# Performance work log

Hardware: AMD Instinct MI355X
Metric: run time of the kernel (lower is better)

Reference implementation:

```python
import jax, jax.numpy as jnp
import numpy as np

TEMPERATURE = 0.8
TOP_K = 50
TOP_P = 0.9
REP_PENALTY = 1.2
NEG_INF = -1000000000.0


def setup_inputs() -> dict:
    key = jax.random.key(0)
    k1, k2 = jax.random.split(key)
    B, S, V, L = 64, 8, 50257, 2048
    logits = jax.random.normal(k1, (B, S, V), dtype=jnp.float32)
    input_ids = jax.random.randint(k2, (B, L), 0, V, dtype=jnp.int64)
    return {"logits": logits, "input_ids": input_ids}


def _modify_logits(logits, input_ids):
    B, S, V = logits.shape
    # temperature scale
    x = logits / TEMPERATURE
    # top-k: keep values >= k-th largest (ties negligible for random floats)
    kth = jax.lax.top_k(x, TOP_K)[0][..., -1:]  # [B,S,1]
    x = jnp.where(x >= kth, x, NEG_INF)
    # top-p nucleus filtering
    order = jnp.argsort(-x, axis=-1)                       # descending order indices
    sorted_logits = jnp.take_along_axis(x, order, axis=-1)
    cum = jnp.cumsum(jax.nn.softmax(sorted_logits, axis=-1), axis=-1)
    remove = cum > TOP_P
    # shift right by one; always keep the top token
    remove = jnp.concatenate([jnp.zeros_like(remove[..., :1]), remove[..., :-1]], axis=-1)
    inv = jnp.argsort(order, axis=-1)                      # inverse permutation
    remove_orig = jnp.take_along_axis(remove, inv, axis=-1)
    x = jnp.where(remove_orig, NEG_INF, x)
    # repetition penalty on last position only, for tokens present in history
    present = jnp.zeros((B, V), dtype=bool).at[
        jnp.arange(B)[:, None], input_ids
    ].set(True)
    last = x[:, -1, :]
    penalized = jnp.where(last < 0, last * REP_PENALTY, last / REP_PENALTY)
    last = jnp.where(present, penalized, last)
    return x.at[:, -1, :].set(last)


def reference(logits, input_ids):
    return _modify_logits(logits, input_ids)
```

## Files before the change

kernel.cpp:

```cpp
#include <hip/hip_runtime.h>
#include <stdint.h>

#define V 50257
#define B_ 64
#define S_ 8
#define ROWS (B_ * S_)
#define L_ 2048
#define NEG_INF -1000000000.0f
#define PEN_NEG (-1200000000.0f)
#define MASK_WORDS_PER_B 1571
#define TOTAL (ROWS * V)
#define NVEC (TOTAL / 4)
#define TOP_CAP 64
#define TRAW 2.8f
#define GBLK_F4 1571
#define GBLOCKS_G ((NVEC + GBLK_F4 - 1) / GBLK_F4)
#define GCAP_BLK 64
#define CAPROW 512

#define WS_BCNT    0
#define WS_GCAND   16384
#define WS_NEED    (WS_GCAND + (size_t)GBLOCKS_G * GCAP_BLK * 8)
#define WS_ROWPARAM 0
#define WS_MASK     8192

__device__ __forceinline__ unsigned fkey(float f) {
    unsigned u = __float_as_uint(f);
    return (u & 0x80000000u) ? ~u : (u | 0x80000000u);
}

__device__ __forceinline__ int blockReduceSum256(int v, int tid, int* s4) {
#pragma unroll
    for (int off = 32; off; off >>= 1) v += __shfl_down(v, off);
    __syncthreads();
    if ((tid & 63) == 0) s4[tid >> 6] = v;
    __syncthreads();
    return s4[0] + s4[1] + s4[2] + s4[3];
}


__global__ __launch_bounds__(256) void prep_kernel(const float4* __restrict__ in4,
                                                   uint2* __restrict__ gcand,
                                                   unsigned* __restrict__ bcnt) {
    const int blk = blockIdx.x;
    const int tid = threadIdx.x;
    const int start = blk * GBLK_F4;
    const int end = min(start + GBLK_F4, NVEC);

    __shared__ uint2 buf[GCAP_BLK];
    __shared__ int lcnt, s_of;
    if (tid == 0) { lcnt = 0; s_of = 0; }
    __syncthreads();

    const int i0 = start + tid;
    const float4* p0 = in4 + min(i0,            NVEC - 1);
    const float4* p1 = in4 + min(i0 + 256,      NVEC - 1);
    const float4* p2 = in4 + min(i0 + 2 * 256,  NVEC - 1);
    const float4* p3 = in4 + min(i0 + 3 * 256,  NVEC - 1);
    const float4* p4 = in4 + min(i0 + 4 * 256,  NVEC - 1);
    const float4* p5 = in4 + min(i0 + 5 * 256,  NVEC - 1);
    const float4* p6 = in4 + min(i0 + 6 * 256,  NVEC - 1);

    float4 va0, va1, va2, va3, va4, va5, va6;
    asm volatile("global_load_dwordx4 %0, %1, off" : "=v"(va0) : "v"(p0));
    asm volatile("global_load_dwordx4 %0, %1, off" : "=v"(va1) : "v"(p1));
    asm volatile("global_load_dwordx4 %0, %1, off" : "=v"(va2) : "v"(p2));
    asm volatile("global_load_dwordx4 %0, %1, off" : "=v"(va3) : "v"(p3));
    asm volatile("global_load_dwordx4 %0, %1, off" : "=v"(va4) : "v"(p4));
    asm volatile("global_load_dwordx4 %0, %1, off" : "=v"(va5) : "v"(p5));
    asm volatile("global_load_dwordx4 %0, %1, off" : "=v"(va6) : "v"(p6));

    asm volatile("s_waitcnt vmcnt(0)" ::: "memory");
    __builtin_amdgcn_sched_barrier(0);

    float c0v = 0.f, c1v = 0.f, c2v = 0.f, c3v = 0.f, c4v = 0.f;
    int c0i = 0, c1i = 0, c2i = 0, c3i = 0, c4i = 0;
    int nh = 0;

#define INS(val, ei)                                                          \
    if ((val) >= TRAW) {                                                      \
        c4v = c3v; c4i = c3i; c3v = c2v; c3i = c2i; c2v = c1v; c2i = c1i;     \
        c1v = c0v; c1i = c0i; c0v = (val); c0i = (ei); ++nh;                  \
    }
#define CONSUME(vv, kk)                                                       \
    {                                                                         \
        int i = i0 + (kk) * 256;                                              \
        if (i < end) {                                                        \
            int e = i << 2;                                                   \
            INS((vv).x, e)                                                    \
            INS((vv).y, e + 1)                                                \
            INS((vv).z, e + 2)                                                \
            INS((vv).w, e + 3)                                                \
        }                                                                     \
    }
    CONSUME(va0, 0) CONSUME(va1, 1) CONSUME(va2, 2) CONSUME(va3, 3)
    CONSUME(va4, 4) CONSUME(va5, 5) CONSUME(va6, 6)
#undef CONSUME
#undef INS

    if (nh > 0) {
        int m = nh > 5 ? 5 : nh;
        if (nh > 5) s_of = 1;
        int base = atomicAdd(&lcnt, m);
        if (m >= 1 && base + 0 < GCAP_BLK) buf[base + 0] = make_uint2((unsigned)c0i, __float_as_uint(c0v));
        if (m >= 2 && base + 1 < GCAP_BLK) buf[base + 1] = make_uint2((unsigned)c1i, __float_as_uint(c1v));
        if (m >= 3 && base + 2 < GCAP_BLK) buf[base + 2] = make_uint2((unsigned)c2i, __float_as_uint(c2v));
        if (m >= 4 && base + 3 < GCAP_BLK) buf[base + 3] = make_uint2((unsigned)c3i, __float_as_uint(c3v));
        if (m >= 5 && base + 4 < GCAP_BLK) buf[base + 4] = make_uint2((unsigned)c4i, __float_as_uint(c4v));
    }
    __syncthreads();
    if (tid == 0) bcnt[blk] = s_of ? 1000000u : (unsigned)lcnt;
    int take = min(lcnt, GCAP_BLK);
    for (int j = tid; j < take; j += 256) gcand[(size_t)blk * GCAP_BLK + j] = buf[j];
}


__global__ __launch_bounds__(256) void select_kernel(const float* __restrict__ logits,
                                                     const int* __restrict__ ids,
                                                     const uint2* __restrict__ gcand,
                                                     const unsigned* __restrict__ bcnt,
                                                     float* __restrict__ out) {
    const int row = blockIdx.x;
    const int tid = threadIdx.x;
    __shared__ float cX[CAPROW];
    __shared__ unsigned cR[CAPROW];
    __shared__ int cI[CAPROW];
    __shared__ float sVal[TOP_CAP];
    __shared__ int sIdx[TOP_CAP];
    __shared__ double sExp[TOP_CAP];
    __shared__ unsigned presRow[MASK_WORDS_PER_B];
    __shared__ int s_c, s_M, s_bad, s_ti;
    __shared__ float s_t;
    __shared__ int s_red[4];

    const float* rp = logits + (size_t)row * V;
    const unsigned e0 = (unsigned)row * (unsigned)V;
    if (tid == 0) { s_c = 0; s_bad = 0; }
    __syncthreads();

    {
        const int b0 = (int)((e0 >> 2) / GBLK_F4);
        const int b1 = (int)(((e0 + V - 1) >> 2) / GBLK_F4);
        for (int blk = b0; blk <= b1; ++blk) {
            unsigned c = bcnt[blk];
            if (c > GCAP_BLK && tid == 0) s_bad = 1;
            int take = min((int)c, GCAP_BLK);
            for (int j = tid; j < take; j += 256) {
                uint2 u = gcand[(size_t)blk * GCAP_BLK + j];
                if (u.x / (unsigned)V == (unsigned)row) {
                    int p = atomicAdd(&s_c, 1);
                    if (p < CAPROW) {
                        cR[p] = u.y;
                        cX[p] = __uint_as_float(u.y) / 0.8f;
                        cI[p] = (int)(u.x - e0);
                    }
                }
            }
        }
    }
    __syncthreads();
    int cnt = s_c;
    if (s_bad || cnt < 50 || cnt > CAPROW) {
        unsigned lo = 0u, hi = 0xFFFFFFFFu;
        while (lo < hi) {
            unsigned mid = lo + ((hi - lo) >> 1) + 1u;
            int c = 0;
            for (int j = tid; j < V; j += 256) c += (int)(fkey(rp[j]) >= mid);
            c = blockReduceSum256(c, tid, s_red);
            if (c >= 50) lo = mid; else hi = mid - 1u;
        }
        unsigned gl = (lo > 2u) ? lo - 2u : 0u;
        __syncthreads();
        if (tid == 0) s_c = 0;
        __syncthreads();
        for (int j = tid; j < V; j += 256) {
            float v = rp[j];
            if (fkey(v) >= gl) {
                int p = atomicAdd(&s_c, 1);
                if (p < CAPROW) { cR[p] = __float_as_uint(v); cX[p] = v / 0.8f; cI[p] = j; }
            }
        }
        __syncthreads();
        cnt = min(s_c, CAPROW);
    }

    if (tid < TOP_CAP) { sVal[tid] = -3.4e38f; sIdx[tid] = 0x7FFFFFFF; }
    __syncthreads();

    {
        float v0 = -3.4e38f, v1 = -3.4e38f;
        int i0 = 0x7FFFFFFF, i1 = 0x7FFFFFFF;
        if (tid < cnt) { v0 = cX[tid]; i0 = cI[tid]; }
        if (tid + 256 < cnt) { v1 = cX[tid + 256]; i1 = cI[tid + 256]; }
        int r0 = 0, r1 = 0;
        for (int j = 0; j < cnt; ++j) {
            float w = cX[j];
            int wi = cI[j];
            r0 += (w > v0) || (w == v0 && wi < i0);
            r1 += (w > v1) || (w == v1 && wi < i1);
        }
        if (tid < cnt && r0 < TOP_CAP) { sVal[r0] = v0; sIdx[r0] = i0; }
        if (tid + 256 < cnt && r1 < TOP_CAP) { sVal[r1] = v1; sIdx[r1] = i1; }
    }
    __syncthreads();

    if (tid == 0) {
        float kth = sVal[49];
        int M = 50;
        while (M < TOP_CAP && sVal[M] == kth) ++M;
        s_M = M;
    }
    __syncthreads();
    int M = s_M;
    if (tid < M) sExp[tid] = exp((double)sVal[tid] - (double)sVal[0]);
    __syncthreads();
    if (tid == 0) {
        double denom = 0.0;
        for (int i = 0; i < M; ++i) denom += sExp[i];
        double cum = 0.0;
        int J = M - 1;
        for (int i = 0; i < M; ++i) {
            cum += sExp[i] / denom;
            if (cum > 0.9) { J = i; break; }
        }
        s_t = sVal[J];
        s_ti = sIdx[J];
    }

    const bool pen = (row & 7) == 7;
    if (pen) {
        __syncthreads();
        for (int w = tid; w < MASK_WORDS_PER_B; w += 256) presRow[w] = 0u;
        __syncthreads();
        const int* bp = ids + (row >> 3) * L_;
#pragma unroll
        for (int k = 0; k < L_ / 256; ++k) {
            int t = bp[k * 256 + tid];
            atomicOr(&presRow[t >> 5], 1u << (t & 31));
        }
    }
    __syncthreads();

    float* orow = out + (size_t)row * V;
    const unsigned mis = (unsigned)(((size_t)row * (size_t)V) & 3u);
    const int a0 = (int)((4u - mis) & 3u);
    const int nv = (V - a0) >> 2;
    const int tailStart = a0 + (nv << 2);
    if (tid < a0) {
        int t = tid;
        orow[t] = (pen && ((presRow[t >> 5] >> (t & 31)) & 1u)) ? PEN_NEG : NEG_INF;
    }
    if (tid < V - tailStart) {
        int t = tailStart + tid;
        orow[t] = (pen && ((presRow[t >> 5] >> (t & 31)) & 1u)) ? PEN_NEG : NEG_INF;
    }
    float4* ob = reinterpret_cast<float4*>(orow + a0);
    if (!pen) {
        const float4 bg = make_float4(NEG_INF, NEG_INF, NEG_INF, NEG_INF);
        for (int j = tid; j < nv; j += 256) ob[j] = bg;
    } else {
        for (int j = tid; j < nv; j += 256) {
            int t = a0 + (j << 2);
            float4 bg;
            bg.x = ((presRow[t >> 5]       >> (t & 31))       & 1u) ? PEN_NEG : NEG_INF;
            bg.y = ((presRow[(t+1) >> 5]   >> ((t+1) & 31))   & 1u) ? PEN_NEG : NEG_INF;
            bg.z = ((presRow[(t+2) >> 5]   >> ((t+2) & 31))   & 1u) ? PEN_NEG : NEG_INF;
            bg.w = ((presRow[(t+3) >> 5]   >> ((t+3) & 31))   & 1u) ? PEN_NEG : NEG_INF;
            ob[j] = bg;
        }
    }
    __syncthreads();

    float t = s_t;
    int tie = s_ti;
    for (int j = tid; j < cnt; j += 256) {
        float x = cX[j];
        int tok = cI[j];
        bool keep = (x > t) || (x == t && tok <= tie);
        if (keep) {
            float oo = x;
            if (pen && ((presRow[tok >> 5] >> (tok & 31)) & 1u))
                oo = (oo < 0.0f) ? oo * 1.2f : oo * (1.0f / 1.2f);
            orow[tok] = oo;
        }
    }
}

#define CAND_CAP 4096
#define RT_THREADS 1024

__global__ __launch_bounds__(256) void mask_only_kernel(const int* __restrict__ ids,
                                                        unsigned* __restrict__ mask) {
    const int tid = threadIdx.x;
    const int b = blockIdx.x;
    __shared__ unsigned lds[MASK_WORDS_PER_B];
    for (int w = tid; w < MASK_WORDS_PER_B; w += 256) lds[w] = 0u;
    __syncthreads();
    const int* bp = ids + b * L_;
#pragma unroll
    for (int k = 0; k < L_ / 256; ++k) {
        int t = bp[k * 256 + tid];
        atomicOr(&lds[t >> 5], 1u << (t & 31));
    }
    __syncthreads();
    unsigned* mp = mask + b * MASK_WORDS_PER_B;
    for (int w = tid; w < MASK_WORDS_PER_B; w += 256) mp[w] = lds[w];
}

__global__ __launch_bounds__(RT_THREADS, 8) void row_thresh_kernel(
        const float* __restrict__ logits, uint4* __restrict__ rowParam) {
    const int tid = threadIdx.x;
    const int row = blockIdx.x;
    if (row >= ROWS) return;
    const float* rp = logits + (size_t)row * V;

    __shared__ float candV[CAND_CAP];
    __shared__ int   candI[CAND_CAP];
    __shared__ float sVal[TOP_CAP];
    __shared__ int   sIdx[TOP_CAP];
    __shared__ double sExp[TOP_CAP];
    __shared__ int s_cnt, s_M;
    __shared__ int s_red[RT_THREADS / 64];

    const unsigned mis = (unsigned)(((size_t)row * (size_t)V) & 3u);
    const int a0 = (int)((4u - mis) & 3u);
    const int nv = (V - a0) >> 2;
    const int tailStart = a0 + (nv << 2);
    const float4* vp = reinterpret_cast<const float4*>(rp + a0);

    float TR = 2.4f;
    int cnt = 0;
    for (int attempt = 0; attempt < 12; ++attempt) {
        if (tid == 0) s_cnt = 0;
        __syncthreads();
        for (int base = tid; base < nv; base += 4 * RT_THREADS) {
            int i1 = base + RT_THREADS, i2 = base + 2 * RT_THREADS, i3 = base + 3 * RT_THREADS;
            float4 a = vp[base];
            float4 b = vp[i1 < nv ? i1 : nv - 1];
            float4 c = vp[i2 < nv ? i2 : nv - 1];
            float4 d = vp[i3 < nv ? i3 : nv - 1];
            float va[16] = {a.x, a.y, a.z, a.w, b.x, b.y, b.z, b.w,
                            c.x, c.y, c.z, c.w, d.x, d.y, d.z, d.w};
            int ib[4] = {base, i1, i2, i3};
            bool ok[4] = {true, i1 < nv, i2 < nv, i3 < nv};
#pragma unroll
            for (int q = 0; q < 4; ++q) {
                if (!ok[q]) continue;
#pragma unroll
                for (int cc = 0; cc < 4; ++cc) {
                    float v = va[q * 4 + cc];
                    if (v >= TR) {
                        int p = atomicAdd(&s_cnt, 1);
                        if (p < CAND_CAP) { candV[p] = v / 0.8f; candI[p] = a0 + (ib[q] << 2) + cc; }
                    }
                }
            }
        }
        if (tid < a0) {
            float v = rp[tid];
            if (v >= TR) {
                int p = atomicAdd(&s_cnt, 1);
                if (p < CAND_CAP) { candV[p] = v / 0.8f; candI[p] = tid; }
            }
        }
        if (tid < V - tailStart) {
            float v = rp[tailStart + tid];
            if (v >= TR) {
                int p = atomicAdd(&s_cnt, 1);
                if (p < CAND_CAP) { candV[p] = v / 0.8f; candI[p] = tailStart + tid; }
            }
        }
        __syncthreads();
        cnt = s_cnt;
        if (cnt >= 50 && cnt <= CAND_CAP) break;
        if (cnt < 50) TR -= 1.2f; else TR += 1.2f;
        __syncthreads();
    }
    if (cnt > CAND_CAP) cnt = CAND_CAP;

    if (tid < TOP_CAP) { sVal[tid] = -3.4e38f; sIdx[tid] = 0x7FFFFFFF; }
    __syncthreads();

    {
        float v0 = (tid < cnt) ? candV[tid] : -3.4e38f;
        int i0 = (tid < cnt) ? candI[tid] : 0x7FFFFFFF;
        float v1 = (tid + RT_THREADS < cnt) ? candV[tid + RT_THREADS] : -3.4e38f;
        int i1 = (tid + RT_THREADS < cnt) ? candI[tid + RT_THREADS] : 0x7FFFFFFF;
        float v2 = (tid + 2 * RT_THREADS < cnt) ? candV[tid + 2 * RT_THREADS] : -3.4e38f;
        int i2 = (tid + 2 * RT_THREADS < cnt) ? candI[tid + 2 * RT_THREADS] : 0x7FFFFFFF;
        float v3 = (tid + 3 * RT_THREADS < cnt) ? candV[tid + 3 * RT_THREADS] : -3.4e38f;
        int i3 = (tid + 3 * RT_THREADS < cnt) ? candI[tid + 3 * RT_THREADS] : 0x7FFFFFFF;
        int r0 = 0, r1 = 0, r2 = 0, r3 = 0;
        for (int j = 0; j < cnt; ++j) {
            float w = candV[j];
            int wi = candI[j];
            r0 += (w > v0) || (w == v0 && wi < i0);
            r1 += (w > v1) || (w == v1 && wi < i1);
            r2 += (w > v2) || (w == v2 && wi < i2);
            r3 += (w > v3) || (w == v3 && wi < i3);
        }
        if (tid < cnt && r0 < TOP_CAP) { sVal[r0] = v0; sIdx[r0] = i0; }
        if (tid + RT_THREADS < cnt && r1 < TOP_CAP) { sVal[r1] = v1; sIdx[r1] = i1; }
        if (tid + 2 * RT_THREADS < cnt && r2 < TOP_CAP) { sVal[r2] = v2; sIdx[r2] = i2; }
        if (tid + 3 * RT_THREADS < cnt && r3 < TOP_CAP) { sVal[r3] = v3; sIdx[r3] = i3; }
    }
    __syncthreads();

    if (tid == 0) {
        float kth = sVal[49];
        int M = 50;
        while (M < TOP_CAP && sVal[M] == kth) ++M;
        s_M = M;
    }
    __syncthreads();
    int M = s_M;
    if (tid < M) sExp[tid] = exp((double)sVal[tid] - (double)sVal[0]);
    __syncthreads();

    if (tid == 0) {
        double denom = 0.0;
#pragma unroll 1
        for (int i = 0; i < M; ++i) denom += sExp[i];
        double cum = 0.0;
        int J = M - 1;
#pragma unroll 1
        for (int i = 0; i < M; ++i) {
            cum += sExp[i] / denom;
            if (cum > 0.9) { J = i; break; }
        }
        float t = sVal[J];
        float w = t * 0.8f;
        unsigned wb = __float_as_uint(w);
        unsigned lo = 0xFFFFFFFFu, hi = 0u;
        for (int d = -4; d <= 4; ++d) {
            unsigned ub = wb + (unsigned)d;
            if (__uint_as_float(ub) / 0.8f == t) { if (ub < lo) lo = ub; if (ub > hi) hi = ub; }
        }
        rowParam[row] = make_uint4(lo, hi, (unsigned)sIdx[J], 0u);
    }
}

__global__ __launch_bounds__(256) void apply_kernel(const float4* __restrict__ in4,
                                                    const uint4* __restrict__ rowParam,
                                                    const unsigned* __restrict__ mask,
                                                    float4* __restrict__ out4) {
    int gid = blockIdx.x * 256 + threadIdx.x;
    int i0 = gid << 1;
    if (i0 >= NVEC) return;
    float4 a = in4[i0];
    float4 b = in4[i0 + 1];
    unsigned e = (unsigned)i0 << 2;
    unsigned row = e / (unsigned)V;
    unsigned tok0 = e - row * (unsigned)V;
    uint4 p0 = rowParam[row];
    bool crosses = (tok0 + 7u >= (unsigned)V);
    uint4 p1 = crosses ? rowParam[row + 1] : p0;
    float xs[8] = {a.x, a.y, a.z, a.w, b.x, b.y, b.z, b.w};
    float o[8];
#pragma unroll
    for (int c = 0; c < 8; ++c) {
        unsigned tok = tok0 + (unsigned)c;
        unsigned r = row;
        uint4 pp = p0;
        if (tok >= (unsigned)V) { tok -= (unsigned)V; r = row + 1u; pp = p1; }
        float v = xs[c];
        float vlo = __uint_as_float(pp.x);
        float vhi = __uint_as_float(pp.y);
        bool keep = (v > vhi) || (v >= vlo && tok <= pp.z);
        float oo = keep ? v * 1.25f : NEG_INF;
        if ((r & 7u) == 7u) {
            unsigned w = mask[(r >> 3) * MASK_WORDS_PER_B + (tok >> 5)];
            if ((w >> (tok & 31u)) & 1u) oo = (oo < 0.0f) ? oo * 1.2f : oo * (1.0f / 1.2f);
        }
        o[c] = oo;
    }
    out4[i0] = make_float4(o[0], o[1], o[2], o[3]);
    out4[i0 + 1] = make_float4(o[4], o[5], o[6], o[7]);
}

extern "C" void kernel_launch(void* const* d_in, const int* in_sizes, int n_in,
                              void* d_out, int out_size, void* d_ws, size_t ws_size,
                              hipStream_t stream) {
    const float* logits = (const float*)d_in[0];
    const int* ids = (const int*)d_in[1];
    float* out = (float*)d_out;

    if (ws_size >= WS_NEED) {
        unsigned* bcnt = (unsigned*)((char*)d_ws + WS_BCNT);
        uint2* gcand = (uint2*)((char*)d_ws + WS_GCAND);
        prep_kernel<<<GBLOCKS_G, 256, 0, stream>>>((const float4*)logits, gcand, bcnt);
        select_kernel<<<ROWS, 256, 0, stream>>>(logits, ids, gcand, bcnt, out);
    } else {
        uint4* rowParam = (uint4*)((char*)d_ws + WS_ROWPARAM);
        unsigned* mask = (unsigned*)((char*)d_ws + WS_MASK);
        mask_only_kernel<<<B_, 256, 0, stream>>>(ids, mask);
        row_thresh_kernel<<<ROWS, RT_THREADS, 0, stream>>>(logits, rowParam);
        apply_kernel<<<(NVEC / 2 + 255) / 256, 256, 0, stream>>>((const float4*)logits, rowParam,
                                                                 mask, (float4*)out);
    }
}
```

Baseline: 57.46 us.

## Replace block-level candidate gather with per-wave chunks and shuffle prefix scan

The threshold prefilter now assigns each wavefront its own contiguous chunk and compacts candidates with a wave-level shuffle prefix sum, writing directly to global memory with a per-wave count. This removes the shared-memory atomics, the block barrier and the staging copy of the previous block-wide gather. The select kernel reads the per-wave counts into shared memory and scans candidate slots in one flattened loop. The cost is more count entries and slots to scan per row, with a smaller per-wave cap (32) that may trigger the slow fallback more often.

```diff
diff --git a/kernel.cpp b/kernel.cpp
--- a/kernel.cpp
+++ b/kernel.cpp
@@ -13,14 +13,17 @@
 #define NVEC (TOTAL / 4)
 #define TOP_CAP 64
 #define TRAW 2.8f
-#define GBLK_F4 1571
-#define GBLOCKS_G ((NVEC + GBLK_F4 - 1) / GBLK_F4)
-#define GCAP_BLK 64
+#define F4L 7
+#define WCHUNK_F4 (64 * F4L)
+#define ELEMS_PER_WAVE (WCHUNK_F4 * 4)
+#define NWAVES ((NVEC + WCHUNK_F4 - 1) / WCHUNK_F4)
+#define GW_BLOCKS ((NWAVES + 3) / 4)
+#define WCAP 32
 #define CAPROW 512
 
-#define WS_BCNT    0
-#define WS_GCAND   16384
-#define WS_NEED    (WS_GCAND + (size_t)GBLOCKS_G * GCAP_BLK * 8)
+#define WS_WCNT    0
+#define WS_GCAND   65536
+#define WS_NEED    (WS_GCAND + (size_t)NWAVES * WCAP * 8)
 #define WS_ROWPARAM 0
 #define WS_MASK     8192
 
@@ -39,53 +42,46 @@
 }
 
 
-__global__ __launch_bounds__(256) void prep_kernel(const float4* __restrict__ in4,
-                                                   uint2* __restrict__ gcand,
-                                                   unsigned* __restrict__ bcnt) {
-    const int blk = blockIdx.x;
-    const int tid = threadIdx.x;
-    const int start = blk * GBLK_F4;
-    const int end = min(start + GBLK_F4, NVEC);
-
-    __shared__ uint2 buf[GCAP_BLK];
-    __shared__ int lcnt, s_of;
-    if (tid == 0) { lcnt = 0; s_of = 0; }
-    __syncthreads();
-
-    const int i0 = start + tid;
-    const float4* p0 = in4 + min(i0,            NVEC - 1);
-    const float4* p1 = in4 + min(i0 + 256,      NVEC - 1);
-    const float4* p2 = in4 + min(i0 + 2 * 256,  NVEC - 1);
-    const float4* p3 = in4 + min(i0 + 3 * 256,  NVEC - 1);
-    const float4* p4 = in4 + min(i0 + 4 * 256,  NVEC - 1);
-    const float4* p5 = in4 + min(i0 + 5 * 256,  NVEC - 1);
-    const float4* p6 = in4 + min(i0 + 6 * 256,  NVEC - 1);
+__global__ __launch_bounds__(256) void gather_kernel(const float4* __restrict__ in4,
+                                                     uint2* __restrict__ gcand,
+                                                     unsigned* __restrict__ wcnt) {
+    const int wid = blockIdx.x * 4 + (threadIdx.x >> 6);
+    if (wid >= NWAVES) return;
+    const int lane = threadIdx.x & 63;
+    const int b = wid * WCHUNK_F4 + lane;
+
+    const float4* p0 = in4 + min(b,          NVEC - 1);
+    const float4* p1 = in4 + min(b + 64,     NVEC - 1);
+    const float4* p2 = in4 + min(b + 2 * 64, NVEC - 1);
+    const float4* p3 = in4 + min(b + 3 * 64, NVEC - 1);
+    const float4* p4 = in4 + min(b + 4 * 64, NVEC - 1);
+    const float4* p5 = in4 + min(b + 5 * 64, NVEC - 1);
+    const float4* p6 = in4 + min(b + 6 * 64, NVEC - 1);
 
     float4 va0, va1, va2, va3, va4, va5, va6;
-    asm volatile("global_load_dwordx4 %0, %1, off" : "=v"(va0) : "v"(p0));
-    asm volatile("global_load_dwordx4 %0, %1, off" : "=v"(va1) : "v"(p1));
-    asm volatile("global_load_dwordx4 %0, %1, off" : "=v"(va2) : "v"(p2));
-    asm volatile("global_load_dwordx4 %0, %1, off" : "=v"(va3) : "v"(p3));
-    asm volatile("global_load_dwordx4 %0, %1, off" : "=v"(va4) : "v"(p4));
-    asm volatile("global_load_dwordx4 %0, %1, off" : "=v"(va5) : "v"(p5));
-    asm volatile("global_load_dwordx4 %0, %1, off" : "=v"(va6) : "v"(p6));
-
+#define LOADPIN(dst, src)                                                     \
+    asm volatile("global_load_dwordx4 %0, %1, off" : "=v"(dst) : "v"(src));   \
+    __builtin_amdgcn_sched_barrier(0);
+    LOADPIN(va0, p0) LOADPIN(va1, p1) LOADPIN(va2, p2) LOADPIN(va3, p3)
+    LOADPIN(va4, p4) LOADPIN(va5, p5) LOADPIN(va6, p6)
+#undef LOADPIN
     asm volatile("s_waitcnt vmcnt(0)" ::: "memory");
     __builtin_amdgcn_sched_barrier(0);
 
-    float c0v = 0.f, c1v = 0.f, c2v = 0.f, c3v = 0.f, c4v = 0.f;
-    int c0i = 0, c1i = 0, c2i = 0, c3i = 0, c4i = 0;
+    float q0v = 0.f, q1v = 0.f, q2v = 0.f, q3v = 0.f, q4v = 0.f, q5v = 0.f, q6v = 0.f, q7v = 0.f;
+    int q0i = 0, q1i = 0, q2i = 0, q3i = 0, q4i = 0, q5i = 0, q6i = 0, q7i = 0;
     int nh = 0;
 
 #define INS(val, ei)                                                          \
     if ((val) >= TRAW) {                                                      \
-        c4v = c3v; c4i = c3i; c3v = c2v; c3i = c2i; c2v = c1v; c2i = c1i;     \
-        c1v = c0v; c1i = c0i; c0v = (val); c0i = (ei); ++nh;                  \
+        q7v = q6v; q7i = q6i; q6v = q5v; q6i = q5i; q5v = q4v; q5i = q4i;     \
+        q4v = q3v; q4i = q3i; q3v = q2v; q3i = q2i; q2v = q1v; q2i = q1i;     \
+        q1v = q0v; q1i = q0i; q0v = (val); q0i = (ei); ++nh;                  \
     }
 #define CONSUME(vv, kk)                                                       \
     {                                                                         \
-        int i = i0 + (kk) * 256;                                              \
-        if (i < end) {                                                        \
+        int i = b + (kk) * 64;                                                \
+        if (i < NVEC) {                                                       \
             int e = i << 2;                                                   \
             INS((vv).x, e)                                                    \
             INS((vv).y, e + 1)                                                \
@@ -98,27 +94,34 @@
 #undef CONSUME
 #undef INS
 
-    if (nh > 0) {
-        int m = nh > 5 ? 5 : nh;
-        if (nh > 5) s_of = 1;
-        int base = atomicAdd(&lcnt, m);
-        if (m >= 1 && base + 0 < GCAP_BLK) buf[base + 0] = make_uint2((unsigned)c0i, __float_as_uint(c0v));
-        if (m >= 2 && base + 1 < GCAP_BLK) buf[base + 1] = make_uint2((unsigned)c1i, __float_as_uint(c1v));
-        if (m >= 3 && base + 2 < GCAP_BLK) buf[base + 2] = make_uint2((unsigned)c2i, __float_as_uint(c2v));
-        if (m >= 4 && base + 3 < GCAP_BLK) buf[base + 3] = make_uint2((unsigned)c3i, __float_as_uint(c3v));
-        if (m >= 5 && base + 4 < GCAP_BLK) buf[base + 4] = make_uint2((unsigned)c4i, __float_as_uint(c4v));
-    }
-    __syncthreads();
-    if (tid == 0) bcnt[blk] = s_of ? 1000000u : (unsigned)lcnt;
-    int take = min(lcnt, GCAP_BLK);
-    for (int j = tid; j < take; j += 256) gcand[(size_t)blk * GCAP_BLK + j] = buf[j];
+    int m = nh > 8 ? 8 : nh;
+    int incl = m;
+#pragma unroll
+    for (int d = 1; d < 64; d <<= 1) {
+        int t = __shfl_up(incl, d);
+        if (lane >= d) incl += t;
+    }
+    int excl = incl - m;
+    int total = __shfl(incl, 63);
+    bool of = (total > WCAP) || __any(nh > 8);
+
+    size_t rb = (size_t)wid * WCAP;
+    if (m >= 1 && excl + 0 < WCAP) gcand[rb + excl + 0] = make_uint2((unsigned)q0i, __float_as_uint(q0v));
+    if (m >= 2 && excl + 1 < WCAP) gcand[rb + excl + 1] = make_uint2((unsigned)q1i, __float_as_uint(q1v));
+    if (m >= 3 && excl + 2 < WCAP) gcand[rb + excl + 2] = make_uint2((unsigned)q2i, __float_as_uint(q2v));
+    if (m >= 4 && excl + 3 < WCAP) gcand[rb + excl + 3] = make_uint2((unsigned)q3i, __float_as_uint(q3v));
+    if (m >= 5 && excl + 4 < WCAP) gcand[rb + excl + 4] = make_uint2((unsigned)q4i, __float_as_uint(q4v));
+    if (m >= 6 && excl + 5 < WCAP) gcand[rb + excl + 5] = make_uint2((unsigned)q5i, __float_as_uint(q5v));
+    if (m >= 7 && excl + 6 < WCAP) gcand[rb + excl + 6] = make_uint2((unsigned)q6i, __float_as_uint(q6v));
+    if (m >= 8 && excl + 7 < WCAP) gcand[rb + excl + 7] = make_uint2((unsigned)q7i, __float_as_uint(q7v));
+    if (lane == 0) wcnt[wid] = of ? 1000000u : (unsigned)total;
 }
 
 
 __global__ __launch_bounds__(256) void select_kernel(const float* __restrict__ logits,
                                                      const int* __restrict__ ids,
                                                      const uint2* __restrict__ gcand,
-                                                     const unsigned* __restrict__ bcnt,
+                                                     const unsigned* __restrict__ wcnt,
                                                      float* __restrict__ out) {
     const int row = blockIdx.x;
     const int tid = threadIdx.x;
@@ -129,6 +132,7 @@
     __shared__ int sIdx[TOP_CAP];
     __shared__ double sExp[TOP_CAP];
     __shared__ unsigned presRow[MASK_WORDS_PER_B];
+    __shared__ unsigned s_wc[40];
     __shared__ int s_c, s_M, s_bad, s_ti;
     __shared__ float s_t;
     __shared__ int s_red[4];
@@ -139,14 +143,19 @@
     __syncthreads();
 
     {
-        const int b0 = (int)((e0 >> 2) / GBLK_F4);
-        const int b1 = (int)(((e0 + V - 1) >> 2) / GBLK_F4);
-        for (int blk = b0; blk <= b1; ++blk) {
-            unsigned c = bcnt[blk];
-            if (c > GCAP_BLK && tid == 0) s_bad = 1;
-            int take = min((int)c, GCAP_BLK);
-            for (int j = tid; j < take; j += 256) {
-                uint2 u = gcand[(size_t)blk * GCAP_BLK + j];
+        const int r0 = (int)(e0 / (unsigned)ELEMS_PER_WAVE);
+        const int r1 = (int)((e0 + V - 1) / (unsigned)ELEMS_PER_WAVE);
+        const int nr = r1 - r0 + 1;
+        if (tid < nr) s_wc[tid] = wcnt[r0 + tid];
+        __syncthreads();
+        const int nslots = nr * WCAP;
+        for (int j = tid; j < nslots; j += 256) {
+            int r = j >> 5;
+            int sl = j & 31;
+            unsigned c = s_wc[r];
+            if (c > (unsigned)WCAP) { s_bad = 1; c = WCAP; }
+            if (sl < (int)c) {
+                uint2 u = gcand[(size_t)(r0 + r) * WCAP + sl];
                 if (u.x / (unsigned)V == (unsigned)row) {
                     int p = atomicAdd(&s_c, 1);
                     if (p < CAPROW) {
@@ -262,10 +271,10 @@
         for (int j = tid; j < nv; j += 256) {
             int t = a0 + (j << 2);
             float4 bg;
-            bg.x = ((presRow[t >> 5]       >> (t & 31))       & 1u) ? PEN_NEG : NEG_INF;
-            bg.y = ((presRow[(t+1) >> 5]   >> ((t+1) & 31))   & 1u) ? PEN_NEG : NEG_INF;
-            bg.z = ((presRow[(t+2) >> 5]   >> ((t+2) & 31))   & 1u) ? PEN_NEG : NEG_INF;
-            bg.w = ((presRow[(t+3) >> 5]   >> ((t+3) & 31))   & 1u) ? PEN_NEG : NEG_INF;
+            bg.x = ((presRow[t >> 5]     >> (t & 31))     & 1u) ? PEN_NEG : NEG_INF;
+            bg.y = ((presRow[(t+1) >> 5] >> ((t+1) & 31)) & 1u) ? PEN_NEG : NEG_INF;
+            bg.z = ((presRow[(t+2) >> 5] >> ((t+2) & 31)) & 1u) ? PEN_NEG : NEG_INF;
+            bg.w = ((presRow[(t+3) >> 5] >> ((t+3) & 31)) & 1u) ? PEN_NEG : NEG_INF;
             ob[j] = bg;
         }
     }
@@ -486,10 +495,10 @@
     float* out = (float*)d_out;
 
     if (ws_size >= WS_NEED) {
-        unsigned* bcnt = (unsigned*)((char*)d_ws + WS_BCNT);
+        unsigned* wcnt = (unsigned*)((char*)d_ws + WS_WCNT);
         uint2* gcand = (uint2*)((char*)d_ws + WS_GCAND);
-        prep_kernel<<<GBLOCKS_G, 256, 0, stream>>>((const float4*)logits, gcand, bcnt);
-        select_kernel<<<ROWS, 256, 0, stream>>>(logits, ids, gcand, bcnt, out);
+        gather_kernel<<<GW_BLOCKS, 256, 0, stream>>>((const float4*)logits, gcand, wcnt);
+        select_kernel<<<ROWS, 256, 0, stream>>>(logits, ids, gcand, wcnt, out);
     } else {
         uint4* rowParam = (uint4*)((char*)d_ws + WS_ROWPARAM);
         unsigned* mask = (unsigned*)((char*)d_ws + WS_MASK);
```

Result: faster. 54.00 us, median of 2 (-6.0%).
